# Performance work log

Hardware: AMD Instinct MI355X
Metric: run time of the kernel (lower is better)

## Reference

```python
import jax, jax.numpy as jnp
import numpy as np

N = 100000   # nodes
E = 1200000  # edges
D = 64       # in_channels == out_channels, heads=1
NEG_SLOPE = 0.2  # PyG GATv2Conv default negative_slope


def setup_inputs() -> dict:
    key = jax.random.key(0)
    k1, k2, k3, k4 = jax.random.split(key, 4)
    x = jax.random.normal(k1, (N, D), dtype=jnp.float32)
    edge_index = jax.random.randint(k2, (2, E), 0, N, dtype=jnp.int32)
    # glorot-ish scale for shared linear (share_weights=True -> lin_l == lin_r)
    W = jax.random.normal(k3, (D, D), dtype=jnp.float32) * (1.0 / np.sqrt(D))
    b = jnp.zeros((D,), dtype=jnp.float32)
    att = jax.random.normal(k4, (D,), dtype=jnp.float32) * (1.0 / np.sqrt(D))
    return {"x": x, "edge_index": edge_index, "W": W, "b": b, "att": att}


def reference(x, edge_index, W, b, att):
    src = edge_index[0]  # source j (messages flow j -> i)
    dst = edge_index[1]  # target i
    # shared linear transform (share_weights=True)
    z = x @ W.T + b                                   # [N, D]
    # GATv2 score: att . leakyrelu(z_j + z_i)
    e = jax.nn.leaky_relu(z[src] + z[dst], NEG_SLOPE) @ att  # [E]
    # segment softmax over incoming edges of each target node
    m = jax.ops.segment_max(e, dst, num_segments=N)   # [N]
    ex = jnp.exp(e - m[dst])                          # [E]
    s = jax.ops.segment_sum(ex, dst, num_segments=N)  # [N]
    alpha = ex / s[dst]                               # [E]
    # SimpleConv(aggr='sum') with edge_weight=alpha on ORIGINAL x
    out = jax.ops.segment_sum(alpha[:, None] * x[src], dst, num_segments=N)  # [N, D]
    return out
```

## Files before the change

### kernel.cpp

```cpp
#include <hip/hip_runtime.h>

#define D 64
#define LOG2E 1.4426950408889634f

using frag_ab = __attribute__((ext_vector_type(8))) short;
using f32x4   = __attribute__((ext_vector_type(4))) float;

__device__ __forceinline__ unsigned short f2bf(float f) {
    unsigned int bits = __float_as_uint(f);
    return (unsigned short)((bits + 0x7fffu + ((bits >> 16) & 1u)) >> 16);
}

__device__ __forceinline__ frag_ab pack8(float4 a, float4 b) {
    frag_ab f;
    f[0] = (short)f2bf(a.x); f[1] = (short)f2bf(a.y);
    f[2] = (short)f2bf(a.z); f[3] = (short)f2bf(a.w);
    f[4] = (short)f2bf(b.x); f[5] = (short)f2bf(b.y);
    f[6] = (short)f2bf(b.z); f[7] = (short)f2bf(b.w);
    return f;
}

__global__ __launch_bounds__(256) void gemm_z_count(const float* __restrict__ x,
                                                    const float* __restrict__ W,
                                                    const float* __restrict__ b,
                                                    unsigned int* __restrict__ zxb,
                                                    int n,
                                                    const int* __restrict__ dst,
                                                    int* __restrict__ deg,
                                                    int* __restrict__ slot,
                                                    int e_cnt) {
    __shared__ float xs[64 * 68];
    int tid = threadIdx.x;

    int gtid = blockIdx.x * 256 + tid;
    int nthreads = gridDim.x * 256;
    int e0 = -1, e1 = -1, e2 = -1, s0 = 0, s1 = 0, s2 = 0;
    {
        int ee = gtid;
        if (ee < e_cnt) { e0 = ee; s0 = atomicAdd(&deg[dst[ee]], 1); ee += nthreads; }
        if (ee < e_cnt) { e1 = ee; s1 = atomicAdd(&deg[dst[ee]], 1); ee += nthreads; }
        if (ee < e_cnt) { e2 = ee; s2 = atomicAdd(&deg[dst[ee]], 1); }
    }

    int row0 = blockIdx.x * 64;
    for (int i = tid; i < 64 * 16; i += 256) {
        int r = i >> 4;
        int gr = row0 + r;
        float4 v = (gr < n) ? ((const float4*)x)[(size_t)gr * 16 + (i & 15)]
                            : make_float4(0.f, 0.f, 0.f, 0.f);
        *(float4*)&xs[r * 68 + (i & 15) * 4] = v;
    }

    int l  = tid & 63;
    int w  = tid >> 6;
    int lr = l & 15;
    int hi = l >> 4;
    int lk = hi * 8;

    frag_ab bfr[4][2];
#pragma unroll
    for (int colt = 0; colt < 4; ++colt) {
#pragma unroll
        for (int ks = 0; ks < 2; ++ks) {
            const float* wp = W + (colt * 16 + lr) * 64 + ks * 32 + lk;
            bfr[colt][ks] = pack8(*(const float4*)wp, *(const float4*)(wp + 4));
        }
    }

    __syncthreads();

    frag_ab afr[2];
#pragma unroll
    for (int ks = 0; ks < 2; ++ks) {
        const float* ap = &xs[(w * 16 + lr) * 68 + ks * 32 + lk];
        afr[ks] = pack8(*(const float4*)ap, *(const float4*)(ap + 4));
    }

    f32x4 zero = {0.f, 0.f, 0.f, 0.f};
    f32x4 acc[4] = {zero, zero, zero, zero};
#pragma unroll
    for (int ks = 0; ks < 2; ++ks) {
#pragma unroll
        for (int colt = 0; colt < 4; ++colt) {
            acc[colt] = __builtin_amdgcn_mfma_f32_16x16x32_bf16(
                afr[ks], bfr[colt][ks], acc[colt], 0, 0, 0);
        }
    }

#pragma unroll
    for (int colt = 0; colt < 4; ++colt) {
        int col = colt * 16 + lr;
        float bb = b[col];
#pragma unroll
        for (int r = 0; r < 4; ++r) {
            int lrow = w * 16 + hi * 4 + r;
            int row  = row0 + lrow;
            if (row < n) {
                float z  = acc[colt][r] + bb;
                float xv = xs[lrow * 68 + col];
                unsigned int u = (unsigned int)f2bf(z) |
                                 ((unsigned int)f2bf(xv) << 16);
                zxb[(size_t)row * 64 + col] = u;
            }
        }
    }

    if (e0 >= 0) slot[e0] = s0;
    if (e1 >= 0) slot[e1] = s1;
    if (e2 >= 0) slot[e2] = s2;
}

__global__ __launch_bounds__(256) void scan_part(const int* __restrict__ deg,
                                                 int* __restrict__ part, int n) {
    __shared__ int red[256];
    int t = threadIdx.x;
    int i = blockIdx.x * 256 + t;
    red[t] = (i < n) ? deg[i] : 0;
    __syncthreads();
    for (int off = 128; off >= 1; off >>= 1) {
        if (t < off) red[t] += red[t + off];
        __syncthreads();
    }
    if (t == 0) part[blockIdx.x] = red[0];
}

__global__ __launch_bounds__(512) void scan_top(int* __restrict__ part, int B) {
    __shared__ int s[512];
    int t = threadIdx.x;
    int v = (t < B) ? part[t] : 0;
    s[t] = v;
    __syncthreads();
    for (int off = 1; off < 512; off <<= 1) {
        int u = (t >= off) ? s[t - off] : 0;
        __syncthreads();
        s[t] += u;
        __syncthreads();
    }
    if (t < B) part[t] = s[t] - v;
}

__global__ __launch_bounds__(256) void scan_final(const int* __restrict__ deg,
                                                  const int* __restrict__ part,
                                                  int* __restrict__ rowstart, int n) {
    __shared__ int s[256];
    int t = threadIdx.x;
    int i = blockIdx.x * 256 + t;
    int v = (i < n) ? deg[i] : 0;
    s[t] = v;
    __syncthreads();
    for (int off = 1; off < 256; off <<= 1) {
        int u = (t >= off) ? s[t - off] : 0;
        __syncthreads();
        s[t] += u;
        __syncthreads();
    }
    int incl = s[t] + part[blockIdx.x];
    if (i < n) rowstart[i] = incl - v;
    if (i == n - 1) rowstart[n] = incl;
}

__global__ __launch_bounds__(256) void csr_fill_slot(const int* __restrict__ src,
                                                     const int* __restrict__ dst,
                                                     const int* __restrict__ rowstart,
                                                     const int* __restrict__ slot,
                                                     int* __restrict__ srcids, int e_cnt) {
    int e = blockIdx.x * 256 + threadIdx.x;
    if (e >= e_cnt) return;
    srcids[rowstart[dst[e]] + slot[e]] = src[e];
}

__global__ __launch_bounds__(256) void gather4b(const int* __restrict__ srcids,
                                                const int* __restrict__ rowstart,
                                                const unsigned int* __restrict__ zxb,
                                                const float* __restrict__ att,
                                                float* __restrict__ out, int n) {
    int lane = threadIdx.x & 63;
    int node = blockIdx.x * 4 + (threadIdx.x >> 6);
    if (node >= n) return;
    int q = lane & 15;
    int h = lane >> 4;
    int rs = rowstart[node], re = rowstart[node + 1];

    const uint4 zdv = *(const uint4*)(zxb + (size_t)node * 64 + 4 * q);
    float zd0 = __uint_as_float(zdv.x << 16);
    float zd1 = __uint_as_float(zdv.y << 16);
    float zd2 = __uint_as_float(zdv.z << 16);
    float zd3 = __uint_as_float(zdv.w << 16);
    float4 av = *(const float4*)(att + 4 * q);
    float a0 = av.x * LOG2E, a1 = av.y * LOG2E, a2 = av.z * LOG2E, a3 = av.w * LOG2E;

    float ax0 = 0.f, ax1 = 0.f, ax2 = 0.f, ax3 = 0.f, ssum = 0.f;
    for (int e = rs; e < re; e += 8) {
        int e0i = e + h, e1i = e + 4 + h;
        bool l0 = e0i < re, l1 = e1i < re;
        int s0 = l0 ? srcids[e0i] : node;
        int s1 = l1 ? srcids[e1i] : node;
        const uint4 r0 = *(const uint4*)(zxb + (size_t)s0 * 64 + 4 * q);
        const uint4 r1 = *(const uint4*)(zxb + (size_t)s1 * 64 + 4 * q);

        float v0 = __uint_as_float(r0.x << 16) + zd0; v0 = v0 > 0.f ? v0 : 0.2f * v0;
        float v1 = __uint_as_float(r0.y << 16) + zd1; v1 = v1 > 0.f ? v1 : 0.2f * v1;
        float v2 = __uint_as_float(r0.z << 16) + zd2; v2 = v2 > 0.f ? v2 : 0.2f * v2;
        float v3 = __uint_as_float(r0.w << 16) + zd3; v3 = v3 > 0.f ? v3 : 0.2f * v3;
        float p0 = v0 * a0 + v1 * a1 + v2 * a2 + v3 * a3;

        float u0 = __uint_as_float(r1.x << 16) + zd0; u0 = u0 > 0.f ? u0 : 0.2f * u0;
        float u1 = __uint_as_float(r1.y << 16) + zd1; u1 = u1 > 0.f ? u1 : 0.2f * u1;
        float u2 = __uint_as_float(r1.z << 16) + zd2; u2 = u2 > 0.f ? u2 : 0.2f * u2;
        float u3 = __uint_as_float(r1.w << 16) + zd3; u3 = u3 > 0.f ? u3 : 0.2f * u3;
        float p1 = u0 * a0 + u1 * a1 + u2 * a2 + u3 * a3;

#pragma unroll
        for (int off = 8; off >= 1; off >>= 1) {
            p0 += __shfl_xor(p0, off, 64);
            p1 += __shfl_xor(p1, off, 64);
        }
        float ex0 = l0 ? __builtin_exp2f(p0) : 0.f;
        float ex1 = l1 ? __builtin_exp2f(p1) : 0.f;
        ssum += ex0 + ex1;
        ax0 += ex0 * __uint_as_float(r0.x & 0xffff0000u)
             + ex1 * __uint_as_float(r1.x & 0xffff0000u);
        ax1 += ex0 * __uint_as_float(r0.y & 0xffff0000u)
             + ex1 * __uint_as_float(r1.y & 0xffff0000u);
        ax2 += ex0 * __uint_as_float(r0.z & 0xffff0000u)
             + ex1 * __uint_as_float(r1.z & 0xffff0000u);
        ax3 += ex0 * __uint_as_float(r0.w & 0xffff0000u)
             + ex1 * __uint_as_float(r1.w & 0xffff0000u);
    }
    ssum += __shfl_xor(ssum, 16, 64); ssum += __shfl_xor(ssum, 32, 64);
    ax0  += __shfl_xor(ax0, 16, 64);  ax0  += __shfl_xor(ax0, 32, 64);
    ax1  += __shfl_xor(ax1, 16, 64);  ax1  += __shfl_xor(ax1, 32, 64);
    ax2  += __shfl_xor(ax2, 16, 64);  ax2  += __shfl_xor(ax2, 32, 64);
    ax3  += __shfl_xor(ax3, 16, 64);  ax3  += __shfl_xor(ax3, 32, 64);
    if (h == 0) {
        float inv = (re > rs) ? 1.f / ssum : 0.f;
        float4 o = make_float4(ax0 * inv, ax1 * inv, ax2 * inv, ax3 * inv);
        *(float4*)&out[(size_t)node * D + 4 * q] = o;
    }
}

extern "C" void kernel_launch(void* const* d_in, const int* in_sizes, int n_in,
                              void* d_out, int out_size, void* d_ws, size_t ws_size,
                              hipStream_t stream) {
    const float* x   = (const float*)d_in[0];
    const int*   ei  = (const int*)d_in[1];
    const float* W   = (const float*)d_in[2];
    const float* b   = (const float*)d_in[3];
    const float* att = (const float*)d_in[4];
    int n = in_sizes[0] / D;
    int e = in_sizes[1] / 2;
    const int* src = ei;
    const int* dst = ei + e;
    float* out = (float*)d_out;

    int nBlkN = (n + 255) / 256;
    int gemmBlk = (n + 63) / 64;

    unsigned int* zxb = (unsigned int*)d_ws;
    int* deg      = (int*)(zxb + (size_t)n * 64);
    int* rowstart = deg + n;
    int* srcids   = rowstart + n + 1;
    int* slot     = srcids + e;
    int* part     = slot + e;

    hipMemsetAsync(deg, 0, (size_t)n * sizeof(int), stream);
    gemm_z_count<<<gemmBlk, 256, 0, stream>>>(x, W, b, zxb, n, dst, deg, slot, e);
    scan_part<<<nBlkN, 256, 0, stream>>>(deg, part, n);
    scan_top<<<1, 512, 0, stream>>>(part, nBlkN);
    scan_final<<<nBlkN, 256, 0, stream>>>(deg, part, rowstart, n);
    csr_fill_slot<<<(e + 255) / 256, 256, 0, stream>>>(src, dst, rowstart, slot, srcids, e);
    gather4b<<<(n + 3) / 4, 256, 0, stream>>>(srcids, rowstart, zxb, att, out, n);
}
```

Before: 230.1 us.

## Build CSR with two-level bucket sort using shared-memory atomics

Replaces the global-atomic degree count, per-edge slot array and scattered CSR fill with a two-pass bucket sort. A block histogram over destination buckets of 256 nodes is scanned, and edges are scattered into bucket order as packed source/low-destination words. A per-bucket kernel then does a local counting sort in shared memory to produce rowstart and srcids. This trades contended, random global atomics and the memset for shared-memory atomics and more coalesced writes. It adds two extra passes over the edge list and assumes source ids fit in 24 bits.

```diff
diff --git a/kernel.cpp b/kernel.cpp
--- a/kernel.cpp
+++ b/kernel.cpp
@@ -2,6 +2,9 @@
 
 #define D 64
 #define LOG2E 1.4426950408889634f
+
+#define HEPT 32
+#define HBLK (256 * HEPT)
 
 using frag_ab = __attribute__((ext_vector_type(8))) short;
 using f32x4   = __attribute__((ext_vector_type(4))) float;
@@ -20,27 +23,13 @@
     return f;
 }
 
-__global__ __launch_bounds__(256) void gemm_z_count(const float* __restrict__ x,
-                                                    const float* __restrict__ W,
-                                                    const float* __restrict__ b,
-                                                    unsigned int* __restrict__ zxb,
-                                                    int n,
-                                                    const int* __restrict__ dst,
-                                                    int* __restrict__ deg,
-                                                    int* __restrict__ slot,
-                                                    int e_cnt) {
+__global__ __launch_bounds__(256) void gemm_z(const float* __restrict__ x,
+                                              const float* __restrict__ W,
+                                              const float* __restrict__ b,
+                                              unsigned int* __restrict__ zxb,
+                                              int n) {
     __shared__ float xs[64 * 68];
     int tid = threadIdx.x;
-
-    int gtid = blockIdx.x * 256 + tid;
-    int nthreads = gridDim.x * 256;
-    int e0 = -1, e1 = -1, e2 = -1, s0 = 0, s1 = 0, s2 = 0;
-    {
-        int ee = gtid;
-        if (ee < e_cnt) { e0 = ee; s0 = atomicAdd(&deg[dst[ee]], 1); ee += nthreads; }
-        if (ee < e_cnt) { e1 = ee; s1 = atomicAdd(&deg[dst[ee]], 1); ee += nthreads; }
-        if (ee < e_cnt) { e2 = ee; s2 = atomicAdd(&deg[dst[ee]], 1); }
-    }
 
     int row0 = blockIdx.x * 64;
     for (int i = tid; i < 64 * 16; i += 256) {
@@ -104,10 +93,23 @@
             }
         }
     }
-
-    if (e0 >= 0) slot[e0] = s0;
-    if (e1 >= 0) slot[e1] = s1;
-    if (e2 >= 0) slot[e2] = s2;
+}
+
+__global__ __launch_bounds__(256) void msd_hist(const int* __restrict__ dst,
+                                                int* __restrict__ hist,
+                                                int e_cnt, int nbuck, int nblk) {
+    __shared__ int cnt[512];
+    int t = threadIdx.x;
+    for (int i = t; i < nbuck; i += 256) cnt[i] = 0;
+    __syncthreads();
+    int base = blockIdx.x * HBLK;
+    for (int j = 0; j < HEPT; ++j) {
+        int e = base + j * 256 + t;
+        if (e < e_cnt) atomicAdd(&cnt[dst[e] >> 8], 1);
+    }
+    __syncthreads();
+    for (int i = t; i < nbuck; i += 256)
+        hist[(size_t)i * nblk + blockIdx.x] = cnt[i];
 }
 
 __global__ __launch_bounds__(256) void scan_part(const int* __restrict__ deg,
@@ -139,13 +141,12 @@
     if (t < B) part[t] = s[t] - v;
 }
 
-__global__ __launch_bounds__(256) void scan_final(const int* __restrict__ deg,
-                                                  const int* __restrict__ part,
-                                                  int* __restrict__ rowstart, int n) {
+__global__ __launch_bounds__(256) void scan_final_ip(int* data,
+                                                     const int* __restrict__ part, int n) {
     __shared__ int s[256];
     int t = threadIdx.x;
     int i = blockIdx.x * 256 + t;
-    int v = (i < n) ? deg[i] : 0;
+    int v = (i < n) ? data[i] : 0;
     s[t] = v;
     __syncthreads();
     for (int off = 1; off < 256; off <<= 1) {
@@ -155,18 +156,70 @@
         __syncthreads();
     }
     int incl = s[t] + part[blockIdx.x];
-    if (i < n) rowstart[i] = incl - v;
-    if (i == n - 1) rowstart[n] = incl;
-}
-
-__global__ __launch_bounds__(256) void csr_fill_slot(const int* __restrict__ src,
-                                                     const int* __restrict__ dst,
-                                                     const int* __restrict__ rowstart,
-                                                     const int* __restrict__ slot,
-                                                     int* __restrict__ srcids, int e_cnt) {
-    int e = blockIdx.x * 256 + threadIdx.x;
-    if (e >= e_cnt) return;
-    srcids[rowstart[dst[e]] + slot[e]] = src[e];
+    if (i < n) data[i] = incl - v;
+    if (i == n - 1) data[n] = incl;
+}
+
+__global__ __launch_bounds__(256) void msd_scatter(const int* __restrict__ src,
+                                                   const int* __restrict__ dst,
+                                                   const int* __restrict__ histS,
+                                                   unsigned int* __restrict__ packed,
+                                                   int e_cnt, int nbuck, int nblk) {
+    __shared__ int cur[512];
+    int t = threadIdx.x;
+    int blk = blockIdx.x;
+    for (int i = t; i < nbuck; i += 256) cur[i] = histS[(size_t)i * nblk + blk];
+    __syncthreads();
+    int base = blk * HBLK;
+    for (int j = 0; j < HEPT; ++j) {
+        int e = base + j * 256 + t;
+        if (e < e_cnt) {
+            int d = dst[e];
+            int s = src[e];
+            int pos = atomicAdd(&cur[d >> 8], 1);
+            packed[pos] = (unsigned int)s | ((unsigned int)(d & 255) << 24);
+        }
+    }
+}
+
+__global__ __launch_bounds__(256) void bucket_csr(const unsigned int* __restrict__ packed,
+                                                  const int* __restrict__ histS,
+                                                  int* __restrict__ rowstart,
+                                                  int* __restrict__ srcids,
+                                                  int n, int e_cnt, int nblk) {
+    __shared__ int cnt[256];
+    __shared__ int s[256];
+    __shared__ int cur[256];
+    int t = threadIdx.x;
+    int b = blockIdx.x;
+    int base = histS[(size_t)b * nblk];
+    int end  = histS[(size_t)(b + 1) * nblk];
+    int m = end - base;
+
+    cnt[t] = 0;
+    __syncthreads();
+    for (int i = t; i < m; i += 256)
+        atomicAdd(&cnt[packed[base + i] >> 24], 1);
+    __syncthreads();
+    s[t] = cnt[t];
+    __syncthreads();
+    for (int off = 1; off < 256; off <<= 1) {
+        int u = (t >= off) ? s[t - off] : 0;
+        __syncthreads();
+        s[t] += u;
+        __syncthreads();
+    }
+    int excl = s[t] - cnt[t];
+    cur[t] = base + excl;
+    int node = (b << 8) + t;
+    if (node < n) rowstart[node] = base + excl;
+    if (b == gridDim.x - 1 && t == 0) rowstart[n] = e_cnt;
+    __syncthreads();
+    for (int i = t; i < m; i += 256) {
+        unsigned int p = packed[base + i];
+        int pos = atomicAdd(&cur[p >> 24], 1);
+        srcids[pos] = (int)(p & 0xFFFFFFu);
+    }
 }
 
 __global__ __launch_bounds__(256) void gather4b(const int* __restrict__ srcids,
@@ -253,21 +306,25 @@
     const int* dst = ei + e;
     float* out = (float*)d_out;
 
-    int nBlkN = (n + 255) / 256;
     int gemmBlk = (n + 63) / 64;
+    int nbuck = (n + 255) >> 8;
+    int nblk1 = (e + HBLK - 1) / HBLK;
+    int NBH   = nbuck * nblk1;
+    int scanBlk = (NBH + 255) / 256;
 
     unsigned int* zxb = (unsigned int*)d_ws;
-    int* deg      = (int*)(zxb + (size_t)n * 64);
-    int* rowstart = deg + n;
+    int* hist     = (int*)(zxb + (size_t)n * 64);
+    int* rowstart = hist + n;
     int* srcids   = rowstart + n + 1;
-    int* slot     = srcids + e;
-    int* part     = slot + e;
-
-    hipMemsetAsync(deg, 0, (size_t)n * sizeof(int), stream);
-    gemm_z_count<<<gemmBlk, 256, 0, stream>>>(x, W, b, zxb, n, dst, deg, slot, e);
-    scan_part<<<nBlkN, 256, 0, stream>>>(deg, part, n);
-    scan_top<<<1, 512, 0, stream>>>(part, nBlkN);
-    scan_final<<<nBlkN, 256, 0, stream>>>(deg, part, rowstart, n);
-    csr_fill_slot<<<(e + 255) / 256, 256, 0, stream>>>(src, dst, rowstart, slot, srcids, e);
+    unsigned int* packed = (unsigned int*)(srcids + e);
+    int* part     = (int*)(packed + e);
+
+    gemm_z<<<gemmBlk, 256, 0, stream>>>(x, W, b, zxb, n);
+    msd_hist<<<nblk1, 256, 0, stream>>>(dst, hist, e, nbuck, nblk1);
+    scan_part<<<scanBlk, 256, 0, stream>>>(hist, part, NBH);
+    scan_top<<<1, 512, 0, stream>>>(part, scanBlk);
+    scan_final_ip<<<scanBlk, 256, 0, stream>>>(hist, part, NBH);
+    msd_scatter<<<nblk1, 256, 0, stream>>>(src, dst, hist, packed, e, nbuck, nblk1);
+    bucket_csr<<<nbuck, 256, 0, stream>>>(packed, hist, rowstart, srcids, n, e, nblk1);
     gather4b<<<(n + 3) / 4, 256, 0, stream>>>(srcids, rowstart, zxb, att, out, n);
 }
```

Measured after the change: 201.2 us. 12.6% less time.

## Build CSR via two-level bucket sort instead of global atomic counting

Applied to the files above, without the earlier changes.

Replaces the per-edge global atomic degree count, three-kernel scan and slot-based fill with a bucketed approach. Edges are grouped into buckets of 128 destination nodes: a shared-memory histogram fused into the GEMM launch, a single-block bucket scan, a block-local scatter into a packed array, then a per-bucket local CSR build in shared memory. This removes contended global atomics and the slot array, at the cost of an extra packed pass. The gather loop also gains an unpredicated main body for full groups of 8 edges and uses fmaxf for leaky ReLU.

```diff
diff --git a/kernel.cpp b/kernel.cpp
--- a/kernel.cpp
+++ b/kernel.cpp
@@ -2,6 +2,9 @@
 
 #define D 64
 #define LOG2E 1.4426950408889634f
+
+#define HEPT_H 8
+#define SEPT 16
 
 using frag_ab = __attribute__((ext_vector_type(8))) short;
 using f32x4   = __attribute__((ext_vector_type(4))) float;
@@ -20,29 +23,35 @@
     return f;
 }
 
-__global__ __launch_bounds__(256) void gemm_z_count(const float* __restrict__ x,
-                                                    const float* __restrict__ W,
-                                                    const float* __restrict__ b,
-                                                    unsigned int* __restrict__ zxb,
-                                                    int n,
-                                                    const int* __restrict__ dst,
-                                                    int* __restrict__ deg,
-                                                    int* __restrict__ slot,
-                                                    int e_cnt) {
+__global__ __launch_bounds__(256) void gemm_z_hist(const float* __restrict__ x,
+                                                   const float* __restrict__ W,
+                                                   const float* __restrict__ b,
+                                                   unsigned int* __restrict__ zxb,
+                                                   int n,
+                                                   const int* __restrict__ dst,
+                                                   int* __restrict__ buckTot,
+                                                   int e_cnt, int histBlk, int nb) {
     __shared__ float xs[64 * 68];
     int tid = threadIdx.x;
 
-    int gtid = blockIdx.x * 256 + tid;
-    int nthreads = gridDim.x * 256;
-    int e0 = -1, e1 = -1, e2 = -1, s0 = 0, s1 = 0, s2 = 0;
-    {
-        int ee = gtid;
-        if (ee < e_cnt) { e0 = ee; s0 = atomicAdd(&deg[dst[ee]], 1); ee += nthreads; }
-        if (ee < e_cnt) { e1 = ee; s1 = atomicAdd(&deg[dst[ee]], 1); ee += nthreads; }
-        if (ee < e_cnt) { e2 = ee; s2 = atomicAdd(&deg[dst[ee]], 1); }
-    }
-
-    int row0 = blockIdx.x * 64;
+    if ((int)blockIdx.x < histBlk) {
+        int* cnt = (int*)xs;
+        for (int i = tid; i < nb; i += 256) cnt[i] = 0;
+        __syncthreads();
+        int base = blockIdx.x * (256 * HEPT_H);
+        for (int j = 0; j < HEPT_H; ++j) {
+            int e = base + j * 256 + tid;
+            if (e < e_cnt) atomicAdd(&cnt[dst[e] >> 7], 1);
+        }
+        __syncthreads();
+        for (int i = tid; i < nb; i += 256) {
+            int c = cnt[i];
+            if (c) atomicAdd(&buckTot[i], c);
+        }
+        return;
+    }
+
+    int row0 = (blockIdx.x - histBlk) * 64;
     for (int i = tid; i < 64 * 16; i += 256) {
         int r = i >> 4;
         int gr = row0 + r;
@@ -104,69 +113,110 @@
             }
         }
     }
-
-    if (e0 >= 0) slot[e0] = s0;
-    if (e1 >= 0) slot[e1] = s1;
-    if (e2 >= 0) slot[e2] = s2;
-}
-
-__global__ __launch_bounds__(256) void scan_part(const int* __restrict__ deg,
-                                                 int* __restrict__ part, int n) {
-    __shared__ int red[256];
+}
+
+__global__ __launch_bounds__(1024) void bucket_scan(const int* __restrict__ buckTot,
+                                                    int* __restrict__ base,
+                                                    int* __restrict__ cursor, int nb) {
+    __shared__ int s[1024];
     int t = threadIdx.x;
-    int i = blockIdx.x * 256 + t;
-    red[t] = (i < n) ? deg[i] : 0;
-    __syncthreads();
-    for (int off = 128; off >= 1; off >>= 1) {
-        if (t < off) red[t] += red[t + off];
-        __syncthreads();
-    }
-    if (t == 0) part[blockIdx.x] = red[0];
-}
-
-__global__ __launch_bounds__(512) void scan_top(int* __restrict__ part, int B) {
-    __shared__ int s[512];
+    int v = (t < nb) ? buckTot[t] : 0;
+    s[t] = v;
+    __syncthreads();
+    for (int off = 1; off < 1024; off <<= 1) {
+        int u = (t >= off) ? s[t - off] : 0;
+        __syncthreads();
+        s[t] += u;
+        __syncthreads();
+    }
+    if (t < nb) {
+        int excl = s[t] - v;
+        base[t]   = excl;
+        cursor[t] = excl;
+    }
+    if (t == nb - 1) base[nb] = s[t];
+}
+
+__global__ __launch_bounds__(256) void msd_scatter(const int* __restrict__ src,
+                                                   const int* __restrict__ dst,
+                                                   int* __restrict__ cursor,
+                                                   unsigned int* __restrict__ packed,
+                                                   int e_cnt, int nb) {
+    __shared__ int es[256 * SEPT];
+    __shared__ int ed[256 * SEPT];
+    __shared__ int cnt[1024];
     int t = threadIdx.x;
-    int v = (t < B) ? part[t] : 0;
-    s[t] = v;
-    __syncthreads();
-    for (int off = 1; off < 512; off <<= 1) {
-        int u = (t >= off) ? s[t - off] : 0;
-        __syncthreads();
-        s[t] += u;
-        __syncthreads();
-    }
-    if (t < B) part[t] = s[t] - v;
-}
-
-__global__ __launch_bounds__(256) void scan_final(const int* __restrict__ deg,
-                                                  const int* __restrict__ part,
-                                                  int* __restrict__ rowstart, int n) {
-    __shared__ int s[256];
+    for (int i = t; i < nb; i += 256) cnt[i] = 0;
+    __syncthreads();
+    int base = blockIdx.x * (256 * SEPT);
+    for (int j = 0; j < SEPT; ++j) {
+        int e = base + j * 256 + t;
+        int idx = j * 256 + t;
+        if (e < e_cnt) {
+            int d = dst[e];
+            es[idx] = src[e];
+            ed[idx] = d;
+            atomicAdd(&cnt[d >> 7], 1);
+        } else {
+            ed[idx] = -1;
+        }
+    }
+    __syncthreads();
+    for (int i = t; i < nb; i += 256) {
+        int c = cnt[i];
+        cnt[i] = c ? atomicAdd(&cursor[i], c) : 0;
+    }
+    __syncthreads();
+    for (int j = 0; j < SEPT; ++j) {
+        int idx = j * 256 + t;
+        int d = ed[idx];
+        if (d >= 0) {
+            int pos = atomicAdd(&cnt[d >> 7], 1);
+            packed[pos] = (unsigned int)es[idx] | ((unsigned int)(d & 127) << 24);
+        }
+    }
+}
+
+__global__ __launch_bounds__(256) void bucket_csr(const unsigned int* __restrict__ packed,
+                                                  const int* __restrict__ base,
+                                                  int* __restrict__ rowstart,
+                                                  int* __restrict__ srcids,
+                                                  int n, int e_cnt, int nb) {
+    __shared__ int cnt[128];
+    __shared__ int sc[128];
+    __shared__ int cur[128];
     int t = threadIdx.x;
-    int i = blockIdx.x * 256 + t;
-    int v = (i < n) ? deg[i] : 0;
-    s[t] = v;
-    __syncthreads();
-    for (int off = 1; off < 256; off <<= 1) {
-        int u = (t >= off) ? s[t - off] : 0;
-        __syncthreads();
-        s[t] += u;
-        __syncthreads();
-    }
-    int incl = s[t] + part[blockIdx.x];
-    if (i < n) rowstart[i] = incl - v;
-    if (i == n - 1) rowstart[n] = incl;
-}
-
-__global__ __launch_bounds__(256) void csr_fill_slot(const int* __restrict__ src,
-                                                     const int* __restrict__ dst,
-                                                     const int* __restrict__ rowstart,
-                                                     const int* __restrict__ slot,
-                                                     int* __restrict__ srcids, int e_cnt) {
-    int e = blockIdx.x * 256 + threadIdx.x;
-    if (e >= e_cnt) return;
-    srcids[rowstart[dst[e]] + slot[e]] = src[e];
+    int b = blockIdx.x;
+    int lo = base[b];
+    int hi = base[b + 1];
+    int m = hi - lo;
+
+    if (t < 128) cnt[t] = 0;
+    __syncthreads();
+    for (int i = t; i < m; i += 256)
+        atomicAdd(&cnt[packed[lo + i] >> 24], 1);
+    __syncthreads();
+    if (t < 128) sc[t] = cnt[t];
+    __syncthreads();
+    for (int off = 1; off < 128; off <<= 1) {
+        int u = (t < 128 && t >= off) ? sc[t - off] : 0;
+        __syncthreads();
+        if (t < 128) sc[t] += u;
+        __syncthreads();
+    }
+    if (t < 128) {
+        int excl = sc[t] - cnt[t];
+        cur[t] = lo + excl;
+        int node = (b << 7) + t;
+        if (node < n) rowstart[node] = lo + excl;
+    }
+    if (b == nb - 1 && t == 0) rowstart[n] = e_cnt;
+    __syncthreads();
+    for (int i = t; i < m; i += 256) {
+        unsigned int p = packed[lo + i];
+        int pos = atomicAdd(&cur[p >> 24], 1);
+        srcids[pos] = (int)(p & 0xFFFFFFu);
+    }
 }
 
 __global__ __launch_bounds__(256) void gather4b(const int* __restrict__ srcids,
@@ -190,7 +240,44 @@
     float a0 = av.x * LOG2E, a1 = av.y * LOG2E, a2 = av.z * LOG2E, a3 = av.w * LOG2E;
 
     float ax0 = 0.f, ax1 = 0.f, ax2 = 0.f, ax3 = 0.f, ssum = 0.f;
-    for (int e = rs; e < re; e += 8) {
+    int efull = rs + ((re - rs) & ~7);
+    int e = rs;
+    for (; e < efull; e += 8) {
+        int s0 = srcids[e + h];
+        int s1 = srcids[e + 4 + h];
+        const uint4 r0 = *(const uint4*)(zxb + (size_t)s0 * 64 + 4 * q);
+        const uint4 r1 = *(const uint4*)(zxb + (size_t)s1 * 64 + 4 * q);
+
+        float v0 = __uint_as_float(r0.x << 16) + zd0; v0 = fmaxf(v0, 0.2f * v0);
+        float v1 = __uint_as_float(r0.y << 16) + zd1; v1 = fmaxf(v1, 0.2f * v1);
+        float v2 = __uint_as_float(r0.z << 16) + zd2; v2 = fmaxf(v2, 0.2f * v2);
+        float v3 = __uint_as_float(r0.w << 16) + zd3; v3 = fmaxf(v3, 0.2f * v3);
+        float p0 = v0 * a0 + v1 * a1 + v2 * a2 + v3 * a3;
+
+        float u0 = __uint_as_float(r1.x << 16) + zd0; u0 = fmaxf(u0, 0.2f * u0);
+        float u1 = __uint_as_float(r1.y << 16) + zd1; u1 = fmaxf(u1, 0.2f * u1);
+        float u2 = __uint_as_float(r1.z << 16) + zd2; u2 = fmaxf(u2, 0.2f * u2);
+        float u3 = __uint_as_float(r1.w << 16) + zd3; u3 = fmaxf(u3, 0.2f * u3);
+        float p1 = u0 * a0 + u1 * a1 + u2 * a2 + u3 * a3;
+
+#pragma unroll
+        for (int off = 8; off >= 1; off >>= 1) {
+            p0 += __shfl_xor(p0, off, 64);
+            p1 += __shfl_xor(p1, off, 64);
+        }
+        float ex0 = __builtin_exp2f(p0);
+        float ex1 = __builtin_exp2f(p1);
+        ssum += ex0 + ex1;
+        ax0 += ex0 * __uint_as_float(r0.x & 0xffff0000u)
+             + ex1 * __uint_as_float(r1.x & 0xffff0000u);
+        ax1 += ex0 * __uint_as_float(r0.y & 0xffff0000u)
+             + ex1 * __uint_as_float(r1.y & 0xffff0000u);
+        ax2 += ex0 * __uint_as_float(r0.z & 0xffff0000u)
+             + ex1 * __uint_as_float(r1.z & 0xffff0000u);
+        ax3 += ex0 * __uint_as_float(r0.w & 0xffff0000u)
+             + ex1 * __uint_as_float(r1.w & 0xffff0000u);
+    }
+    if (e < re) {
         int e0i = e + h, e1i = e + 4 + h;
         bool l0 = e0i < re, l1 = e1i < re;
         int s0 = l0 ? srcids[e0i] : node;
@@ -198,16 +285,16 @@
         const uint4 r0 = *(const uint4*)(zxb + (size_t)s0 * 64 + 4 * q);
         const uint4 r1 = *(const uint4*)(zxb + (size_t)s1 * 64 + 4 * q);
 
-        float v0 = __uint_as_float(r0.x << 16) + zd0; v0 = v0 > 0.f ? v0 : 0.2f * v0;
-        float v1 = __uint_as_float(r0.y << 16) + zd1; v1 = v1 > 0.f ? v1 : 0.2f * v1;
-        float v2 = __uint_as_float(r0.z << 16) + zd2; v2 = v2 > 0.f ? v2 : 0.2f * v2;
-        float v3 = __uint_as_float(r0.w << 16) + zd3; v3 = v3 > 0.f ? v3 : 0.2f * v3;
+        float v0 = __uint_as_float(r0.x << 16) + zd0; v0 = fmaxf(v0, 0.2f * v0);
+        float v1 = __uint_as_float(r0.y << 16) + zd1; v1 = fmaxf(v1, 0.2f * v1);
+        float v2 = __uint_as_float(r0.z << 16) + zd2; v2 = fmaxf(v2, 0.2f * v2);
+        float v3 = __uint_as_float(r0.w << 16) + zd3; v3 = fmaxf(v3, 0.2f * v3);
         float p0 = v0 * a0 + v1 * a1 + v2 * a2 + v3 * a3;
 
-        float u0 = __uint_as_float(r1.x << 16) + zd0; u0 = u0 > 0.f ? u0 : 0.2f * u0;
-        float u1 = __uint_as_float(r1.y << 16) + zd1; u1 = u1 > 0.f ? u1 : 0.2f * u1;
-        float u2 = __uint_as_float(r1.z << 16) + zd2; u2 = u2 > 0.f ? u2 : 0.2f * u2;
-        float u3 = __uint_as_float(r1.w << 16) + zd3; u3 = u3 > 0.f ? u3 : 0.2f * u3;
+        float u0 = __uint_as_float(r1.x << 16) + zd0; u0 = fmaxf(u0, 0.2f * u0);
+        float u1 = __uint_as_float(r1.y << 16) + zd1; u1 = fmaxf(u1, 0.2f * u1);
+        float u2 = __uint_as_float(r1.z << 16) + zd2; u2 = fmaxf(u2, 0.2f * u2);
+        float u3 = __uint_as_float(r1.w << 16) + zd3; u3 = fmaxf(u3, 0.2f * u3);
         float p1 = u0 * a0 + u1 * a1 + u2 * a2 + u3 * a3;
 
 #pragma unroll
@@ -253,21 +340,24 @@
     const int* dst = ei + e;
     float* out = (float*)d_out;
 
-    int nBlkN = (n + 255) / 256;
     int gemmBlk = (n + 63) / 64;
+    int nb      = (n + 127) >> 7;
+    int histBlk = (e + 256 * HEPT_H - 1) / (256 * HEPT_H);
+    int scatBlk = (e + 256 * SEPT - 1) / (256 * SEPT);
 
     unsigned int* zxb = (unsigned int*)d_ws;
-    int* deg      = (int*)(zxb + (size_t)n * 64);
-    int* rowstart = deg + n;
+    int* buckTot  = (int*)(zxb + (size_t)n * 64);
+    int* base     = buckTot + nb;
+    int* cursor   = base + nb + 1;
+    int* rowstart = cursor + nb;
     int* srcids   = rowstart + n + 1;
-    int* slot     = srcids + e;
-    int* part     = slot + e;
-
-    hipMemsetAsync(deg, 0, (size_t)n * sizeof(int), stream);
-    gemm_z_count<<<gemmBlk, 256, 0, stream>>>(x, W, b, zxb, n, dst, deg, slot, e);
-    scan_part<<<nBlkN, 256, 0, stream>>>(deg, part, n);
-    scan_top<<<1, 512, 0, stream>>>(part, nBlkN);
-    scan_final<<<nBlkN, 256, 0, stream>>>(deg, part, rowstart, n);
-    csr_fill_slot<<<(e + 255) / 256, 256, 0, stream>>>(src, dst, rowstart, slot, srcids, e);
+    unsigned int* packed = (unsigned int*)(srcids + e);
+
+    hipMemsetAsync(buckTot, 0, (size_t)nb * sizeof(int), stream);
+    gemm_z_hist<<<histBlk + gemmBlk, 256, 0, stream>>>(x, W, b, zxb, n,
+                                                       dst, buckTot, e, histBlk, nb);
+    bucket_scan<<<1, 1024, 0, stream>>>(buckTot, base, cursor, nb);
+    msd_scatter<<<scatBlk, 256, 0, stream>>>(src, dst, cursor, packed, e, nb);
+    bucket_csr<<<nb, 256, 0, stream>>>(packed, base, rowstart, srcids, n, e, nb);
     gather4b<<<(n + 3) / 4, 256, 0, stream>>>(srcids, rowstart, zxb, att, out, n);
 }
```

Result: faster. 204.0 us (-11.3%).
